# Performance work log

Hardware: AMD Instinct MI355X
Metric: run time of the kernel (lower is better)

The kernel has to match this reference:

```python
import jax, jax.numpy as jnp
import numpy as np

HIDDEN = 64
NUM_LAYERS = 6
BN_EPS = 1e-5


def setup_inputs() -> dict:
    key = jax.random.key(0)
    N, M = 1024, 1024
    num_nodes = N + M
    ks = jax.random.split(key, 12)
    x = jax.random.normal(ks[0], (num_nodes, 2), dtype=jnp.float32)
    # complete bipartite edges: (a, N+b) for all a in [0,N), b in [0,M), row-major so view(N,M) is meaningful
    row = jnp.repeat(jnp.arange(N, dtype=jnp.int64), M)
    col = N + jnp.tile(jnp.arange(M, dtype=jnp.int64), N)
    edge_index = jnp.stack([row, col], axis=0)
    s = 1.0 / np.sqrt(HIDDEN)
    return {
        "x": x,
        "edge_index": edge_index,
        "in_w": jax.random.normal(ks[1], (2, HIDDEN), jnp.float32) * 0.5,
        "in_b": jnp.zeros((HIDDEN,), jnp.float32),
        "conv_w": jax.random.normal(ks[2], (NUM_LAYERS, HIDDEN, HIDDEN), jnp.float32) * s,
        "conv_b": jnp.zeros((NUM_LAYERS, HIDDEN), jnp.float32),
        "bn_gamma": jnp.ones((NUM_LAYERS, HIDDEN), jnp.float32),
        "bn_beta": jnp.zeros((NUM_LAYERS, HIDDEN), jnp.float32),
        "out_w": jax.random.normal(ks[3], (2 * HIDDEN, 1), jnp.float32) * s,
        "out_b": jnp.zeros((1,), jnp.float32),
        "N": N,
        "M": M,
    }


def reference(x, edge_index, in_w, in_b, conv_w, conv_b, bn_gamma, bn_beta, out_w, out_b, N, M):
    num_nodes = x.shape[0]
    # GCN normalization with added self-loops (PyG GCNConv defaults)
    loops = jnp.arange(num_nodes, dtype=edge_index.dtype)
    row = jnp.concatenate([edge_index[0], loops])
    col = jnp.concatenate([edge_index[1], loops])
    deg = jax.ops.segment_sum(jnp.ones_like(col, dtype=x.dtype), col, num_segments=num_nodes)
    dinv = jnp.where(deg > 0, jax.lax.rsqrt(deg), 0.0)
    norm = dinv[row] * dinv[col]  # [E+num_nodes]

    h = jax.nn.relu(x @ in_w + in_b)
    for i in range(NUM_LAYERS):
        h_res = h
        hw = h @ conv_w[i]
        agg = jax.ops.segment_sum(hw[row] * norm[:, None], col, num_segments=num_nodes)
        h = agg + conv_b[i]
        # BatchNorm1d in training mode: batch stats, biased variance
        mu = h.mean(axis=0)
        var = ((h - mu) ** 2).mean(axis=0)
        h = (h - mu) * jax.lax.rsqrt(var + BN_EPS) * bn_gamma[i] + bn_beta[i]
        h = jax.nn.relu(h)
        if i > 0 and i % 2 == 1:
            h = h + h_res

    ef = jnp.concatenate([h[edge_index[0]], h[edge_index[1]]], axis=1)  # [E, 2H]
    scores = (ef @ out_w + out_b)[:, 0]
    return scores.reshape(N, M)
```

## Files before the change

### kernel.cpp

```cpp
#include <hip/hip_runtime.h>


#define NBLK 64
#define MAGIC 0x13572468u

__device__ __forceinline__ float relu_(float x) { return x > 0.f ? x : 0.f; }

#define AT_LOAD(p)    __hip_atomic_load((p), __ATOMIC_RELAXED, __HIP_MEMORY_SCOPE_AGENT)
#define AT_STORE(p,v) __hip_atomic_store((p), (v), __ATOMIC_RELAXED, __HIP_MEMORY_SCOPE_AGENT)
#define AT_ADD(p,v)   __hip_atomic_fetch_add((p), (v), __ATOMIC_RELAXED, __HIP_MEMORY_SCOPE_AGENT)

#define PART_OFF  256
#define UV_OFF    12544
#define FLAG_OFF  14592

__global__ __launch_bounds__(256, 1) void k_fused(
    const float* __restrict__ x,
    const float* __restrict__ in_w, const float* __restrict__ in_b,
    const float* __restrict__ conv_w,
    const float* __restrict__ bn_g, const float* __restrict__ bn_b,
    const float* __restrict__ out_w,
    unsigned int* __restrict__ ws)
{
    __shared__ float Wl[2][4096];
    __shared__ float hl[2048];
    __shared__ float Pp[3 * 2048];
    __shared__ float stat[256];
    __shared__ float g_lds[384], b_lds[384];
    __shared__ float ow_lds[128];

    const int t = threadIdx.x, b = blockIdx.x;
    const int w    = t >> 6;
    const int lane = t & 63;
    const int fi   = lane & 7;
    const int f0   = fi * 8;
    const int ng   = lane >> 3;
    const int n0   = ng * 4;
    const int sw   = ng & 3;
    const int kb   = w * 16;
    const bool isA = b < 32;
    float* part = (float*)(ws + PART_OFF);
    float* uv   = (float*)(ws + UV_OFF);

    {
        const float4* src = (const float4*)conv_w;
        float4* dst = (float4*)Wl[0];
        dst[t]       = src[t];
        dst[t + 256] = src[t + 256];
        dst[t + 512] = src[t + 512];
        dst[t + 768] = src[t + 768];
        for (int i = t; i < 384; i += 256) { g_lds[i] = bn_g[i]; b_lds[i] = bn_b[i]; }
        if (t < 128) ow_lds[t] = out_w[t];
    }

    if (b == 0) {
        for (int i = t; i < 192; i += 256) AT_STORE(ws + i, 0u);
        for (int i = t; i < 12288; i += 256) AT_STORE((unsigned*)part + i, 0u);
        asm volatile("s_waitcnt vmcnt(0)" ::: "memory");
        __syncthreads();
        if (t == 0) AT_STORE(ws + FLAG_OFF, MAGIC);
    }

    {
        const int nl = t >> 3, fj = (t & 7) * 8;
        const int rsw = (nl >> 2) & 3;
        const int node = b * 32 + nl;
        float x0 = x[node * 2], x1 = x[node * 2 + 1];
#pragma unroll
        for (int j = 0; j < 8; j++) {
            int f = fj + j;
            float v = relu_(fmaf(x0, in_w[f], fmaf(x1, in_w[64 + f], in_b[f])));
            hl[nl * 64 + ((((f >> 2)) ^ rsw) << 2) + (f & 3)] = v;
        }
    }
    __syncthreads();

    for (int layer = 0; layer < 6; layer++) {
        const float* Wb = Wl[layer & 1];
        float acc[4][8];
#pragma unroll
        for (int n = 0; n < 4; n++)
#pragma unroll
            for (int j = 0; j < 8; j++) acc[n][j] = 0.f;

#pragma unroll
        for (int kk = 0; kk < 16; kk += 4) {
            const int cb = (kb + kk) >> 2;
            float hv[4][4];
#pragma unroll
            for (int n = 0; n < 4; n++) {
                float4 h4 = *(const float4*)&hl[(n0 + n) * 64 + ((cb ^ sw) << 2)];
                hv[n][0] = h4.x; hv[n][1] = h4.y; hv[n][2] = h4.z; hv[n][3] = h4.w;
            }
#pragma unroll
            for (int j = 0; j < 4; j++) {
                const float* wr = Wb + (kb + kk + j) * 64 + f0;
                float4 w0 = *(const float4*)wr;
                float4 w1 = *(const float4*)(wr + 4);
                float wv[8] = {w0.x, w0.y, w0.z, w0.w, w1.x, w1.y, w1.z, w1.w};
#pragma unroll
                for (int n = 0; n < 4; n++)
#pragma unroll
                    for (int q = 0; q < 8; q++)
                        acc[n][q] = fmaf(hv[n][j], wv[q], acc[n][q]);
            }
        }

        float4 pf0, pf1, pf2, pf3;

        if (w > 0) {
            if (layer < 5) {
                const float4* src = (const float4*)(conv_w + (layer + 1) * 4096);
                pf0 = src[t];
                pf1 = src[t + 256];
                pf2 = src[t + 512];
                pf3 = src[t + 768];
            }
            float* Pw = Pp + (w - 1) * 2048;
#pragma unroll
            for (int n = 0; n < 4; n++) {
                float* prow = Pw + (n0 + n) * 64;
                *(float4*)&prow[((2 * fi)     ^ sw) << 2] =
                    make_float4(acc[n][0], acc[n][1], acc[n][2], acc[n][3]);
                *(float4*)&prow[((2 * fi + 1) ^ sw) << 2] =
                    make_float4(acc[n][4], acc[n][5], acc[n][6], acc[n][7]);
            }
        }
        __syncthreads();

        if (w == 0) {
#pragma unroll
            for (int r = 0; r < 3; r++) {
                const float* Pr = Pp + r * 2048;
#pragma unroll
                for (int n = 0; n < 4; n++) {
                    const float* prow = Pr + (n0 + n) * 64;
                    float4 p0 = *(const float4*)&prow[((2 * fi)     ^ sw) << 2];
                    float4 p1 = *(const float4*)&prow[((2 * fi + 1) ^ sw) << 2];
                    acc[n][0] += p0.x; acc[n][1] += p0.y; acc[n][2] += p0.z; acc[n][3] += p0.w;
                    acc[n][4] += p1.x; acc[n][5] += p1.y; acc[n][6] += p1.z; acc[n][7] += p1.w;
                }
            }
            float sv[8], qv[8];
#pragma unroll
            for (int j = 0; j < 8; j++) {
                sv[j] = (acc[0][j] + acc[1][j]) + (acc[2][j] + acc[3][j]);
                qv[j] = fmaf(acc[0][j], acc[0][j], fmaf(acc[1][j], acc[1][j],
                        fmaf(acc[2][j], acc[2][j], acc[3][j] * acc[3][j])));
            }
#pragma unroll
            for (int m = 8; m < 64; m <<= 1) {
#pragma unroll
                for (int j = 0; j < 8; j++) {
                    sv[j] += __shfl_xor(sv[j], m);
                    qv[j] += __shfl_xor(qv[j], m);
                }
            }
            if (layer == 0) { while (AT_LOAD(ws + FLAG_OFF) != MAGIC) {} }
            if (ng == 0) {
                float* base = part + layer * 2048 + (b & 7) * 256 + (isA ? 0 : 128) + f0;
#pragma unroll
                for (int j = 0; j < 8; j++) {
                    AT_ADD(base + j, sv[j]);
                    AT_ADD(base + 64 + j, qv[j]);
                }
            }
            asm volatile("s_waitcnt vmcnt(0)" ::: "memory");
            if (lane == 0) AT_ADD(ws + layer * 32, 1u);
            if (layer < 5) {
                const float4* src = (const float4*)(conv_w + (layer + 1) * 4096);
                pf0 = src[t];
                pf1 = src[t + 256];
                pf2 = src[t + 512];
                pf3 = src[t + 768];
            }
            if (t == 0) {
                const unsigned int* c = ws + layer * 32;
                for (;;) {
                    unsigned a0 = AT_LOAD(c);
                    unsigned a1 = AT_LOAD(c);
                    unsigned a2 = AT_LOAD(c);
                    unsigned a3 = AT_LOAD(c);
                    if (a0 >= NBLK) break;
                    if (a1 >= NBLK) break;
                    if (a2 >= NBLK) break;
                    if (a3 >= NBLK) break;
                }
            }
        }
        __syncthreads();

        {
            const float* p = part + layer * 2048 + t;
            float s = 0.f;
#pragma unroll
            for (int r = 0; r < 8; r++) s += AT_LOAD(p + r * 256);
            stat[t] = s;
        }
        if (layer < 5) {
            float4* dst = (float4*)Wl[(layer + 1) & 1];
            dst[t]       = pf0;
            dst[t + 256] = pf1;
            dst[t + 512] = pf2;
            dst[t + 768] = pf3;
        }
        __syncthreads();

        if (w == 0) {
            float pc[8], sc[8];
            {
                float4 sa0 = *(const float4*)&stat[f0];
                float4 sa1 = *(const float4*)&stat[f0 + 4];
                float4 qa0 = *(const float4*)&stat[64 + f0];
                float4 qa1 = *(const float4*)&stat[64 + f0 + 4];
                float4 sb0 = *(const float4*)&stat[128 + f0];
                float4 sb1 = *(const float4*)&stat[128 + f0 + 4];
                float4 qb0 = *(const float4*)&stat[192 + f0];
                float4 qb1 = *(const float4*)&stat[192 + f0 + 4];
                float4 gg0 = *(const float4*)&g_lds[layer * 64 + f0];
                float4 gg1 = *(const float4*)&g_lds[layer * 64 + f0 + 4];
                float4 bb0 = *(const float4*)&b_lds[layer * 64 + f0];
                float4 bb1 = *(const float4*)&b_lds[layer * 64 + f0 + 4];
                float SA[8] = {sa0.x, sa0.y, sa0.z, sa0.w, sa1.x, sa1.y, sa1.z, sa1.w};
                float QA[8] = {qa0.x, qa0.y, qa0.z, qa0.w, qa1.x, qa1.y, qa1.z, qa1.w};
                float SB[8] = {sb0.x, sb0.y, sb0.z, sb0.w, sb1.x, sb1.y, sb1.z, sb1.w};
                float QB[8] = {qb0.x, qb0.y, qb0.z, qb0.w, qb1.x, qb1.y, qb1.z, qb1.w};
                float GG[8] = {gg0.x, gg0.y, gg0.z, gg0.w, gg1.x, gg1.y, gg1.z, gg1.w};
                float BB[8] = {bb0.x, bb0.y, bb0.z, bb0.w, bb1.x, bb1.y, bb1.z, bb1.w};
                const float c1 = 9.75609756097561e-4f;
                const float c2 = 3.1234752377721214e-2f;
#pragma unroll
                for (int j = 0; j < 8; j++) {
                    float sumAgg = SA[j] + c1 * SB[j] + 1024.f * c2 * SA[j];
                    float sumSq  = QA[j] + c1 * c1 * QB[j] + 2.f * c1 * c2 * SA[j] * SB[j]
                                 + 1024.f * c2 * c2 * SA[j] * SA[j];
                    float meanAgg = sumAgg * (1.f / 2048.f);
                    float var = sumSq * (1.f / 2048.f) - meanAgg * meanAgg;
                    float rstd = rsqrtf(var + 1e-5f);
                    float scale = rstd * GG[j];
                    if (isA) { pc[j] = scale;      sc[j] = BB[j] - meanAgg * scale; }
                    else     { pc[j] = c1 * scale; sc[j] = BB[j] + (c2 * SA[j] - meanAgg) * scale; }
                }
            }
            float vals[4][8];
#pragma unroll
            for (int n = 0; n < 4; n++)
#pragma unroll
                for (int j = 0; j < 8; j++)
                    vals[n][j] = relu_(fmaf(acc[n][j], pc[j], sc[j]));
            if (layer == 1 || layer == 3 || layer == 5) {
#pragma unroll
                for (int n = 0; n < 4; n++) {
                    const float* hrow = hl + (n0 + n) * 64;
                    float4 r0 = *(const float4*)&hrow[((2 * fi)     ^ sw) << 2];
                    float4 r1 = *(const float4*)&hrow[((2 * fi + 1) ^ sw) << 2];
                    vals[n][0] += r0.x; vals[n][1] += r0.y; vals[n][2] += r0.z; vals[n][3] += r0.w;
                    vals[n][4] += r1.x; vals[n][5] += r1.y; vals[n][6] += r1.z; vals[n][7] += r1.w;
                }
            }
            if (layer < 5) {
#pragma unroll
                for (int n = 0; n < 4; n++) {
                    float* hrow = hl + (n0 + n) * 64;
                    *(float4*)&hrow[((2 * fi)     ^ sw) << 2] =
                        make_float4(vals[n][0], vals[n][1], vals[n][2], vals[n][3]);
                    *(float4*)&hrow[((2 * fi + 1) ^ sw) << 2] =
                        make_float4(vals[n][4], vals[n][5], vals[n][6], vals[n][7]);
                }
            } else {
                const float* wv = ow_lds + (isA ? 0 : 64) + f0;
                float4 o0 = *(const float4*)wv;
                float4 o1 = *(const float4*)(wv + 4);
                float d[4];
#pragma unroll
                for (int n = 0; n < 4; n++) {
                    d[n] = fmaf(vals[n][0], o0.x, fmaf(vals[n][1], o0.y,
                           fmaf(vals[n][2], o0.z, fmaf(vals[n][3], o0.w,
                           fmaf(vals[n][4], o1.x, fmaf(vals[n][5], o1.y,
                           fmaf(vals[n][6], o1.z, vals[n][7] * o1.w)))))));
                    d[n] += __shfl_xor(d[n], 1);
                    d[n] += __shfl_xor(d[n], 2);
                    d[n] += __shfl_xor(d[n], 4);
                }
                if (fi == 0) {
#pragma unroll
                    for (int n = 0; n < 4; n++)
                        AT_STORE(uv + b * 32 + n0 + n, d[n]);
                }
            }
        }
        __syncthreads();
    }
}

__global__ __launch_bounds__(256) void k_out(const float* __restrict__ uv,
                                             const float* __restrict__ out_b,
                                             float* __restrict__ out) {
    const int a = blockIdx.x;
    const int t = threadIdx.x;
    float ua = uv[a] + out_b[0];
    float4 vv = ((const float4*)(uv + 1024))[t];
    ((float4*)(out + a * 1024))[t] =
        make_float4(ua + vv.x, ua + vv.y, ua + vv.z, ua + vv.w);
}

extern "C" void kernel_launch(void* const* d_in, const int* in_sizes, int n_in,
                              void* d_out, int out_size, void* d_ws, size_t ws_size,
                              hipStream_t stream) {
    const float* x      = (const float*)d_in[0];
    const float* in_w   = (const float*)d_in[2];
    const float* in_b   = (const float*)d_in[3];
    const float* conv_w = (const float*)d_in[4];
    const float* bn_g   = (const float*)d_in[6];
    const float* bn_b   = (const float*)d_in[7];
    const float* out_w  = (const float*)d_in[8];
    const float* out_b  = (const float*)d_in[9];
    float* out = (float*)d_out;

    unsigned int* ws = (unsigned int*)d_ws;
    const float* uv = (const float*)(ws + UV_OFF);

    k_fused<<<NBLK, 256, 0, stream>>>(x, in_w, in_b, conv_w, bn_g, bn_b,
                                      out_w, ws);
    k_out<<<1024, 256, 0, stream>>>(uv, out_b, out);
}
```

Baseline: 118.6 us.

## Move grid-barrier stat reduction into wave 0 and spread counters

Reworks the per-layer grid synchronisation so that only wave 0 spins. It polls four spread-out arrival counters while reading the partial BatchNorm sums in the same loop, which removes one block-wide __syncthreads and the shared stat buffer. The per-lane atomic adds are spread across lanes instead of issued serially by one lane group. BN coefficients are computed once per feature and shared through LDS. The next-layer weight prefetch moves entirely to waves 1-3, which store it to LDS while wave 0 waits. The trade-off is heavier polling traffic, since every spin iteration reloads all the partial sums.

```diff
diff --git a/kernel.cpp b/kernel.cpp
--- a/kernel.cpp
+++ b/kernel.cpp
@@ -10,9 +10,9 @@
 #define AT_STORE(p,v) __hip_atomic_store((p), (v), __ATOMIC_RELAXED, __HIP_MEMORY_SCOPE_AGENT)
 #define AT_ADD(p,v)   __hip_atomic_fetch_add((p), (v), __ATOMIC_RELAXED, __HIP_MEMORY_SCOPE_AGENT)
 
-#define PART_OFF  256
-#define UV_OFF    12544
-#define FLAG_OFF  14592
+#define PART_OFF  768
+#define UV_OFF    13056
+#define FLAG_OFF  15104
 
 __global__ __launch_bounds__(256, 1) void k_fused(
     const float* __restrict__ x,
@@ -25,7 +25,7 @@
     __shared__ float Wl[2][4096];
     __shared__ float hl[2048];
     __shared__ float Pp[3 * 2048];
-    __shared__ float stat[256];
+    __shared__ float pcoef[64], scoef[64];
     __shared__ float g_lds[384], b_lds[384];
     __shared__ float ow_lds[128];
 
@@ -54,8 +54,7 @@
     }
 
     if (b == 0) {
-        for (int i = t; i < 192; i += 256) AT_STORE(ws + i, 0u);
-        for (int i = t; i < 12288; i += 256) AT_STORE((unsigned*)part + i, 0u);
+        for (int i = t; i < PART_OFF + 12288; i += 256) AT_STORE(ws + i, 0u);
         asm volatile("s_waitcnt vmcnt(0)" ::: "memory");
         __syncthreads();
         if (t == 0) AT_STORE(ws + FLAG_OFF, MAGIC);
@@ -106,15 +105,14 @@
             }
         }
 
-        float4 pf0, pf1, pf2, pf3;
-
+        float4 pf[6];
+        const int idx = (w - 1) * 64 + lane;
         if (w > 0) {
             if (layer < 5) {
                 const float4* src = (const float4*)(conv_w + (layer + 1) * 4096);
-                pf0 = src[t];
-                pf1 = src[t + 256];
-                pf2 = src[t + 512];
-                pf3 = src[t + 768];
+#pragma unroll
+                for (int r = 0; r < 5; r++) pf[r] = src[idx + 192 * r];
+                if (idx < 64) pf[5] = src[idx + 960];
             }
             float* Pw = Pp + (w - 1) * 2048;
 #pragma unroll
@@ -128,7 +126,14 @@
         }
         __syncthreads();
 
-        if (w == 0) {
+        if (w > 0) {
+            if (layer < 5) {
+                float4* dst = (float4*)Wl[(layer + 1) & 1];
+#pragma unroll
+                for (int r = 0; r < 5; r++) dst[idx + 192 * r] = pf[r];
+                if (idx < 64) dst[idx + 960] = pf[5];
+            }
+        } else {
 #pragma unroll
             for (int r = 0; r < 3; r++) {
                 const float* Pr = Pp + r * 2048;
@@ -157,91 +162,62 @@
                 }
             }
             if (layer == 0) { while (AT_LOAD(ws + FLAG_OFF) != MAGIC) {} }
-            if (ng == 0) {
-                float* base = part + layer * 2048 + (b & 7) * 256 + (isA ? 0 : 128) + f0;
-#pragma unroll
-                for (int j = 0; j < 8; j++) {
-                    AT_ADD(base + j, sv[j]);
-                    AT_ADD(base + 64 + j, qv[j]);
-                }
+
+            {
+                float* base = part + layer * 2048 + (b & 7) * 256 + (isA ? 0 : 128);
+                AT_ADD(base + f0 + ng, sv[ng]);
+                AT_ADD(base + 64 + f0 + ng, qv[ng]);
             }
             asm volatile("s_waitcnt vmcnt(0)" ::: "memory");
-            if (lane == 0) AT_ADD(ws + layer * 32, 1u);
-            if (layer < 5) {
-                const float4* src = (const float4*)(conv_w + (layer + 1) * 4096);
-                pf0 = src[t];
-                pf1 = src[t + 256];
-                pf2 = src[t + 512];
-                pf3 = src[t + 768];
-            }
-            if (t == 0) {
-                const unsigned int* c = ws + layer * 32;
+            if (lane == 0) AT_ADD(ws + layer * 128 + (b & 3) * 32, 1u);
+
+            float SA, QA, SB, QB;
+            {
+                const float* p = part + layer * 2048 + lane;
+                const unsigned int* c = ws + layer * 128;
                 for (;;) {
-                    unsigned a0 = AT_LOAD(c);
-                    unsigned a1 = AT_LOAD(c);
-                    unsigned a2 = AT_LOAD(c);
-                    unsigned a3 = AT_LOAD(c);
-                    if (a0 >= NBLK) break;
-                    if (a1 >= NBLK) break;
-                    if (a2 >= NBLK) break;
-                    if (a3 >= NBLK) break;
-                }
-            }
-        }
-        __syncthreads();
-
-        {
-            const float* p = part + layer * 2048 + t;
-            float s = 0.f;
-#pragma unroll
-            for (int r = 0; r < 8; r++) s += AT_LOAD(p + r * 256);
-            stat[t] = s;
-        }
-        if (layer < 5) {
-            float4* dst = (float4*)Wl[(layer + 1) & 1];
-            dst[t]       = pf0;
-            dst[t + 256] = pf1;
-            dst[t + 512] = pf2;
-            dst[t + 768] = pf3;
-        }
-        __syncthreads();
-
-        if (w == 0) {
+                    unsigned c0 = AT_LOAD(c);
+                    unsigned c1 = AT_LOAD(c + 32);
+                    unsigned c2 = AT_LOAD(c + 64);
+                    unsigned c3 = AT_LOAD(c + 96);
+                    float a0 = 0.f, a1 = 0.f, a2 = 0.f, a3 = 0.f;
+#pragma unroll
+                    for (int r = 0; r < 8; r++) {
+                        a0 += AT_LOAD(p + r * 256);
+                        a1 += AT_LOAD(p + r * 256 + 64);
+                        a2 += AT_LOAD(p + r * 256 + 128);
+                        a3 += AT_LOAD(p + r * 256 + 192);
+                    }
+                    if (c0 + c1 + c2 + c3 == NBLK) { SA = a0; QA = a1; SB = a2; QB = a3; break; }
+                }
+            }
+
+            {
+                const float c1 = 9.75609756097561e-4f;
+                const float c2 = 3.1234752377721214e-2f;
+                float sumAgg = SA + c1 * SB + 1024.f * c2 * SA;
+                float sumSq  = QA + c1 * c1 * QB + 2.f * c1 * c2 * SA * SB
+                             + 1024.f * c2 * c2 * SA * SA;
+                float meanAgg = sumAgg * (1.f / 2048.f);
+                float var = sumSq * (1.f / 2048.f) - meanAgg * meanAgg;
+                float rstd = rsqrtf(var + 1e-5f);
+                float scale = rstd * g_lds[layer * 64 + lane];
+                float bt = b_lds[layer * 64 + lane];
+                if (isA) { pcoef[lane] = scale;      scoef[lane] = bt - meanAgg * scale; }
+                else     { pcoef[lane] = c1 * scale; scoef[lane] = bt + (c2 * SA - meanAgg) * scale; }
+            }
             float pc[8], sc[8];
             {
-                float4 sa0 = *(const float4*)&stat[f0];
-                float4 sa1 = *(const float4*)&stat[f0 + 4];
-                float4 qa0 = *(const float4*)&stat[64 + f0];
-                float4 qa1 = *(const float4*)&stat[64 + f0 + 4];
-                float4 sb0 = *(const float4*)&stat[128 + f0];
-                float4 sb1 = *(const float4*)&stat[128 + f0 + 4];
-                float4 qb0 = *(const float4*)&stat[192 + f0];
-                float4 qb1 = *(const float4*)&stat[192 + f0 + 4];
-                float4 gg0 = *(const float4*)&g_lds[layer * 64 + f0];
-                float4 gg1 = *(const float4*)&g_lds[layer * 64 + f0 + 4];
-                float4 bb0 = *(const float4*)&b_lds[layer * 64 + f0];
-                float4 bb1 = *(const float4*)&b_lds[layer * 64 + f0 + 4];
-                float SA[8] = {sa0.x, sa0.y, sa0.z, sa0.w, sa1.x, sa1.y, sa1.z, sa1.w};
-                float QA[8] = {qa0.x, qa0.y, qa0.z, qa0.w, qa1.x, qa1.y, qa1.z, qa1.w};
-                float SB[8] = {sb0.x, sb0.y, sb0.z, sb0.w, sb1.x, sb1.y, sb1.z, sb1.w};
-                float QB[8] = {qb0.x, qb0.y, qb0.z, qb0.w, qb1.x, qb1.y, qb1.z, qb1.w};
-                float GG[8] = {gg0.x, gg0.y, gg0.z, gg0.w, gg1.x, gg1.y, gg1.z, gg1.w};
-                float BB[8] = {bb0.x, bb0.y, bb0.z, bb0.w, bb1.x, bb1.y, bb1.z, bb1.w};
-                const float c1 = 9.75609756097561e-4f;
-                const float c2 = 3.1234752377721214e-2f;
-#pragma unroll
-                for (int j = 0; j < 8; j++) {
-                    float sumAgg = SA[j] + c1 * SB[j] + 1024.f * c2 * SA[j];
-                    float sumSq  = QA[j] + c1 * c1 * QB[j] + 2.f * c1 * c2 * SA[j] * SB[j]
-                                 + 1024.f * c2 * c2 * SA[j] * SA[j];
-                    float meanAgg = sumAgg * (1.f / 2048.f);
-                    float var = sumSq * (1.f / 2048.f) - meanAgg * meanAgg;
-                    float rstd = rsqrtf(var + 1e-5f);
-                    float scale = rstd * GG[j];
-                    if (isA) { pc[j] = scale;      sc[j] = BB[j] - meanAgg * scale; }
-                    else     { pc[j] = c1 * scale; sc[j] = BB[j] + (c2 * SA[j] - meanAgg) * scale; }
-                }
-            }
+                float4 p0 = *(const float4*)&pcoef[f0];
+                float4 p1 = *(const float4*)&pcoef[f0 + 4];
+                float4 s0 = *(const float4*)&scoef[f0];
+                float4 s1 = *(const float4*)&scoef[f0 + 4];
+                pc[0] = p0.x; pc[1] = p0.y; pc[2] = p0.z; pc[3] = p0.w;
+                pc[4] = p1.x; pc[5] = p1.y; pc[6] = p1.z; pc[7] = p1.w;
+                sc[0] = s0.x; sc[1] = s0.y; sc[2] = s0.z; sc[3] = s0.w;
+                sc[4] = s1.x; sc[5] = s1.y; sc[6] = s1.z; sc[7] = s1.w;
+            }
+
             float vals[4][8];
 #pragma unroll
             for (int n = 0; n < 4; n++)
```

Measured after the change: 109.9 us (median of 2 runs). -7.3%, faster.

## Replace persistent grid-barrier kernel with per-layer kernel launches

Applied to the files above, without the earlier changes.

Splits the single persistent kernel, which used atomic counters and spin-wait grid barriers between layers, into a chain of kernels: an input kernel, five per-layer kernels, a final kernel and the output kernel. Per-block statistics and pre-BN activations are written to workspace and re-read by the next launch, so no atomics or spinning are needed. The cost is extra kernel launch overhead and global-memory round trips for activations, residuals and weights on every layer.

```diff
diff --git a/kernel.cpp b/kernel.cpp
--- a/kernel.cpp
+++ b/kernel.cpp
@@ -2,295 +2,287 @@
 
 
 #define NBLK 64
-#define MAGIC 0x13572468u
+
+#define ST_OFF   0
+#define ACC_OFF  49152
+#define HB_OFF   180224
+#define UV_OFF   311296
 
 __device__ __forceinline__ float relu_(float x) { return x > 0.f ? x : 0.f; }
 
-#define AT_LOAD(p)    __hip_atomic_load((p), __ATOMIC_RELAXED, __HIP_MEMORY_SCOPE_AGENT)
-#define AT_STORE(p,v) __hip_atomic_store((p), (v), __ATOMIC_RELAXED, __HIP_MEMORY_SCOPE_AGENT)
-#define AT_ADD(p,v)   __hip_atomic_fetch_add((p), (v), __ATOMIC_RELAXED, __HIP_MEMORY_SCOPE_AGENT)
-
-#define PART_OFF  256
-#define UV_OFF    12544
-#define FLAG_OFF  14592
-
-__global__ __launch_bounds__(256, 1) void k_fused(
-    const float* __restrict__ x,
-    const float* __restrict__ in_w, const float* __restrict__ in_b,
-    const float* __restrict__ conv_w,
-    const float* __restrict__ bn_g, const float* __restrict__ bn_b,
-    const float* __restrict__ out_w,
-    unsigned int* __restrict__ ws)
-{
-    __shared__ float Wl[2][4096];
-    __shared__ float hl[2048];
-    __shared__ float Pp[3 * 2048];
-    __shared__ float stat[256];
-    __shared__ float g_lds[384], b_lds[384];
-    __shared__ float ow_lds[128];
-
+__device__ __forceinline__ void gemm_sk(const float* __restrict__ Wb,
+                                        const float* __restrict__ hl,
+                                        int n0, int sw, int kb, int f0,
+                                        float acc[4][8])
+{
+#pragma unroll
+    for (int kk = 0; kk < 16; kk += 4) {
+        const int cb = (kb + kk) >> 2;
+        float hv[4][4];
+#pragma unroll
+        for (int n = 0; n < 4; n++) {
+            float4 h4 = *(const float4*)&hl[(n0 + n) * 64 + ((cb ^ sw) << 2)];
+            hv[n][0] = h4.x; hv[n][1] = h4.y; hv[n][2] = h4.z; hv[n][3] = h4.w;
+        }
+#pragma unroll
+        for (int j = 0; j < 4; j++) {
+            const float* wr = Wb + (kb + kk + j) * 64 + f0;
+            float4 w0 = *(const float4*)wr;
+            float4 w1 = *(const float4*)(wr + 4);
+            float wv[8] = {w0.x, w0.y, w0.z, w0.w, w1.x, w1.y, w1.z, w1.w};
+#pragma unroll
+            for (int n = 0; n < 4; n++)
+#pragma unroll
+                for (int q = 0; q < 8; q++)
+                    acc[n][q] = fmaf(hv[n][j], wv[q], acc[n][q]);
+        }
+    }
+}
+
+__device__ __forceinline__ void publish_layer(float acc[4][8], float* Pp,
+                                              float* st_cur, float* accb,
+                                              int t, int b)
+{
+    const int w = t >> 6, lane = t & 63, fi = lane & 7, f0 = fi * 8;
+    const int ng = lane >> 3, n0 = ng * 4, sw = ng & 3;
+    if (w > 0) {
+        float* Pw = Pp + (w - 1) * 2048;
+#pragma unroll
+        for (int n = 0; n < 4; n++) {
+            float* prow = Pw + (n0 + n) * 64;
+            *(float4*)&prow[((2 * fi)     ^ sw) << 2] =
+                make_float4(acc[n][0], acc[n][1], acc[n][2], acc[n][3]);
+            *(float4*)&prow[((2 * fi + 1) ^ sw) << 2] =
+                make_float4(acc[n][4], acc[n][5], acc[n][6], acc[n][7]);
+        }
+    }
+    __syncthreads();
+    if (w == 0) {
+#pragma unroll
+        for (int r = 0; r < 3; r++) {
+            const float* Pr = Pp + r * 2048;
+#pragma unroll
+            for (int n = 0; n < 4; n++) {
+                const float* prow = Pr + (n0 + n) * 64;
+                float4 p0 = *(const float4*)&prow[((2 * fi)     ^ sw) << 2];
+                float4 p1 = *(const float4*)&prow[((2 * fi + 1) ^ sw) << 2];
+                acc[n][0] += p0.x; acc[n][1] += p0.y; acc[n][2] += p0.z; acc[n][3] += p0.w;
+                acc[n][4] += p1.x; acc[n][5] += p1.y; acc[n][6] += p1.z; acc[n][7] += p1.w;
+            }
+        }
+        float sv[8], qv[8];
+#pragma unroll
+        for (int j = 0; j < 8; j++) {
+            sv[j] = (acc[0][j] + acc[1][j]) + (acc[2][j] + acc[3][j]);
+            qv[j] = fmaf(acc[0][j], acc[0][j], fmaf(acc[1][j], acc[1][j],
+                    fmaf(acc[2][j], acc[2][j], acc[3][j] * acc[3][j])));
+        }
+#pragma unroll
+        for (int m = 8; m < 64; m <<= 1) {
+#pragma unroll
+            for (int j = 0; j < 8; j++) {
+                sv[j] += __shfl_xor(sv[j], m);
+                qv[j] += __shfl_xor(qv[j], m);
+            }
+        }
+        st_cur[b * 128 + f0 + ng]      = sv[ng];
+        st_cur[b * 128 + 64 + f0 + ng] = qv[ng];
+#pragma unroll
+        for (int n = 0; n < 4; n++) {
+            float* arow = accb + (b * 32 + n0 + n) * 64 + f0;
+            *(float4*)arow       = make_float4(acc[n][0], acc[n][1], acc[n][2], acc[n][3]);
+            *(float4*)(arow + 4) = make_float4(acc[n][4], acc[n][5], acc[n][6], acc[n][7]);
+        }
+    }
+}
+
+__device__ __forceinline__ void bn_coefs(const float* stat, int fj, bool isA,
+                                         float4 gg0, float4 gg1,
+                                         float4 bb0, float4 bb1,
+                                         float pc[8], float sc[8])
+{
+    float4 sa0 = *(const float4*)&stat[fj],       sa1 = *(const float4*)&stat[fj + 4];
+    float4 qa0 = *(const float4*)&stat[64 + fj],  qa1 = *(const float4*)&stat[64 + fj + 4];
+    float4 sb0 = *(const float4*)&stat[128 + fj], sb1 = *(const float4*)&stat[128 + fj + 4];
+    float4 qb0 = *(const float4*)&stat[192 + fj], qb1 = *(const float4*)&stat[192 + fj + 4];
+    float SA[8] = {sa0.x, sa0.y, sa0.z, sa0.w, sa1.x, sa1.y, sa1.z, sa1.w};
+    float QA[8] = {qa0.x, qa0.y, qa0.z, qa0.w, qa1.x, qa1.y, qa1.z, qa1.w};
+    float SB[8] = {sb0.x, sb0.y, sb0.z, sb0.w, sb1.x, sb1.y, sb1.z, sb1.w};
+    float QB[8] = {qb0.x, qb0.y, qb0.z, qb0.w, qb1.x, qb1.y, qb1.z, qb1.w};
+    float GG[8] = {gg0.x, gg0.y, gg0.z, gg0.w, gg1.x, gg1.y, gg1.z, gg1.w};
+    float BB[8] = {bb0.x, bb0.y, bb0.z, bb0.w, bb1.x, bb1.y, bb1.z, bb1.w};
+    const float c1 = 9.75609756097561e-4f;
+    const float c2 = 3.1234752377721214e-2f;
+#pragma unroll
+    for (int j = 0; j < 8; j++) {
+        float sumAgg = SA[j] + c1 * SB[j] + 1024.f * c2 * SA[j];
+        float sumSq  = QA[j] + c1 * c1 * QB[j] + 2.f * c1 * c2 * SA[j] * SB[j]
+                     + 1024.f * c2 * c2 * SA[j] * SA[j];
+        float meanAgg = sumAgg * (1.f / 2048.f);
+        float var = sumSq * (1.f / 2048.f) - meanAgg * meanAgg;
+        float rstd = rsqrtf(var + 1e-5f);
+        float scale = rstd * GG[j];
+        if (isA) { pc[j] = scale;      sc[j] = BB[j] - meanAgg * scale; }
+        else     { pc[j] = c1 * scale; sc[j] = BB[j] + (c2 * SA[j] - meanAgg) * scale; }
+    }
+}
+
+__global__ __launch_bounds__(256, 1) void k_in(
+    const float* __restrict__ x, const float* __restrict__ in_w,
+    const float* __restrict__ in_b, const float* __restrict__ conv_w,
+    float* __restrict__ wsf)
+{
+    __shared__ float Wl[4096], hl[2048], Pp[3 * 2048];
     const int t = threadIdx.x, b = blockIdx.x;
-    const int w    = t >> 6;
-    const int lane = t & 63;
-    const int fi   = lane & 7;
-    const int f0   = fi * 8;
-    const int ng   = lane >> 3;
-    const int n0   = ng * 4;
-    const int sw   = ng & 3;
-    const int kb   = w * 16;
-    const bool isA = b < 32;
-    float* part = (float*)(ws + PART_OFF);
-    float* uv   = (float*)(ws + UV_OFF);
-
+    const float4* srcW = (const float4*)conv_w;
+    float4 w0 = srcW[t], w1 = srcW[t + 256], w2 = srcW[t + 512], w3 = srcW[t + 768];
     {
-        const float4* src = (const float4*)conv_w;
-        float4* dst = (float4*)Wl[0];
-        dst[t]       = src[t];
-        dst[t + 256] = src[t + 256];
-        dst[t + 512] = src[t + 512];
-        dst[t + 768] = src[t + 768];
-        for (int i = t; i < 384; i += 256) { g_lds[i] = bn_g[i]; b_lds[i] = bn_b[i]; }
-        if (t < 128) ow_lds[t] = out_w[t];
-    }
-
-    if (b == 0) {
-        for (int i = t; i < 192; i += 256) AT_STORE(ws + i, 0u);
-        for (int i = t; i < 12288; i += 256) AT_STORE((unsigned*)part + i, 0u);
-        asm volatile("s_waitcnt vmcnt(0)" ::: "memory");
-        __syncthreads();
-        if (t == 0) AT_STORE(ws + FLAG_OFF, MAGIC);
-    }
-
-    {
-        const int nl = t >> 3, fj = (t & 7) * 8;
-        const int rsw = (nl >> 2) & 3;
+        const int nl = t >> 3, fj = (t & 7) * 8, rsw = (nl >> 2) & 3;
         const int node = b * 32 + nl;
         float x0 = x[node * 2], x1 = x[node * 2 + 1];
 #pragma unroll
         for (int j = 0; j < 8; j++) {
             int f = fj + j;
             float v = relu_(fmaf(x0, in_w[f], fmaf(x1, in_w[64 + f], in_b[f])));
-            hl[nl * 64 + ((((f >> 2)) ^ rsw) << 2) + (f & 3)] = v;
-        }
-    }
-    __syncthreads();
-
-    for (int layer = 0; layer < 6; layer++) {
-        const float* Wb = Wl[layer & 1];
-        float acc[4][8];
-#pragma unroll
-        for (int n = 0; n < 4; n++)
-#pragma unroll
-            for (int j = 0; j < 8; j++) acc[n][j] = 0.f;
-
-#pragma unroll
-        for (int kk = 0; kk < 16; kk += 4) {
-            const int cb = (kb + kk) >> 2;
-            float hv[4][4];
-#pragma unroll
-            for (int n = 0; n < 4; n++) {
-                float4 h4 = *(const float4*)&hl[(n0 + n) * 64 + ((cb ^ sw) << 2)];
-                hv[n][0] = h4.x; hv[n][1] = h4.y; hv[n][2] = h4.z; hv[n][3] = h4.w;
-            }
-#pragma unroll
-            for (int j = 0; j < 4; j++) {
-                const float* wr = Wb + (kb + kk + j) * 64 + f0;
-                float4 w0 = *(const float4*)wr;
-                float4 w1 = *(const float4*)(wr + 4);
-                float wv[8] = {w0.x, w0.y, w0.z, w0.w, w1.x, w1.y, w1.z, w1.w};
-#pragma unroll
-                for (int n = 0; n < 4; n++)
-#pragma unroll
-                    for (int q = 0; q < 8; q++)
-                        acc[n][q] = fmaf(hv[n][j], wv[q], acc[n][q]);
-            }
-        }
-
-        float4 pf0, pf1, pf2, pf3;
-
-        if (w > 0) {
-            if (layer < 5) {
-                const float4* src = (const float4*)(conv_w + (layer + 1) * 4096);
-                pf0 = src[t];
-                pf1 = src[t + 256];
-                pf2 = src[t + 512];
-                pf3 = src[t + 768];
-            }
-            float* Pw = Pp + (w - 1) * 2048;
-#pragma unroll
-            for (int n = 0; n < 4; n++) {
-                float* prow = Pw + (n0 + n) * 64;
-                *(float4*)&prow[((2 * fi)     ^ sw) << 2] =
-                    make_float4(acc[n][0], acc[n][1], acc[n][2], acc[n][3]);
-                *(float4*)&prow[((2 * fi + 1) ^ sw) << 2] =
-                    make_float4(acc[n][4], acc[n][5], acc[n][6], acc[n][7]);
-            }
-        }
-        __syncthreads();
-
-        if (w == 0) {
-#pragma unroll
-            for (int r = 0; r < 3; r++) {
-                const float* Pr = Pp + r * 2048;
-#pragma unroll
-                for (int n = 0; n < 4; n++) {
-                    const float* prow = Pr + (n0 + n) * 64;
-                    float4 p0 = *(const float4*)&prow[((2 * fi)     ^ sw) << 2];
-                    float4 p1 = *(const float4*)&prow[((2 * fi + 1) ^ sw) << 2];
-                    acc[n][0] += p0.x; acc[n][1] += p0.y; acc[n][2] += p0.z; acc[n][3] += p0.w;
-                    acc[n][4] += p1.x; acc[n][5] += p1.y; acc[n][6] += p1.z; acc[n][7] += p1.w;
-                }
-            }
-            float sv[8], qv[8];
-#pragma unroll
-            for (int j = 0; j < 8; j++) {
-                sv[j] = (acc[0][j] + acc[1][j]) + (acc[2][j] + acc[3][j]);
-                qv[j] = fmaf(acc[0][j], acc[0][j], fmaf(acc[1][j], acc[1][j],
-                        fmaf(acc[2][j], acc[2][j], acc[3][j] * acc[3][j])));
-            }
-#pragma unroll
-            for (int m = 8; m < 64; m <<= 1) {
-#pragma unroll
-                for (int j = 0; j < 8; j++) {
-                    sv[j] += __shfl_xor(sv[j], m);
-                    qv[j] += __shfl_xor(qv[j], m);
-                }
-            }
-            if (layer == 0) { while (AT_LOAD(ws + FLAG_OFF) != MAGIC) {} }
-            if (ng == 0) {
-                float* base = part + layer * 2048 + (b & 7) * 256 + (isA ? 0 : 128) + f0;
-#pragma unroll
-                for (int j = 0; j < 8; j++) {
-                    AT_ADD(base + j, sv[j]);
-                    AT_ADD(base + 64 + j, qv[j]);
-                }
-            }
-            asm volatile("s_waitcnt vmcnt(0)" ::: "memory");
-            if (lane == 0) AT_ADD(ws + layer * 32, 1u);
-            if (layer < 5) {
-                const float4* src = (const float4*)(conv_w + (layer + 1) * 4096);
-                pf0 = src[t];
-                pf1 = src[t + 256];
-                pf2 = src[t + 512];
-                pf3 = src[t + 768];
-            }
-            if (t == 0) {
-                const unsigned int* c = ws + layer * 32;
-                for (;;) {
-                    unsigned a0 = AT_LOAD(c);
-                    unsigned a1 = AT_LOAD(c);
-                    unsigned a2 = AT_LOAD(c);
-                    unsigned a3 = AT_LOAD(c);
-                    if (a0 >= NBLK) break;
-                    if (a1 >= NBLK) break;
-                    if (a2 >= NBLK) break;
-                    if (a3 >= NBLK) break;
-                }
-            }
-        }
-        __syncthreads();
-
-        {
-            const float* p = part + layer * 2048 + t;
-            float s = 0.f;
-#pragma unroll
-            for (int r = 0; r < 8; r++) s += AT_LOAD(p + r * 256);
-            stat[t] = s;
-        }
-        if (layer < 5) {
-            float4* dst = (float4*)Wl[(layer + 1) & 1];
-            dst[t]       = pf0;
-            dst[t + 256] = pf1;
-            dst[t + 512] = pf2;
-            dst[t + 768] = pf3;
-        }
-        __syncthreads();
-
-        if (w == 0) {
-            float pc[8], sc[8];
-            {
-                float4 sa0 = *(const float4*)&stat[f0];
-                float4 sa1 = *(const float4*)&stat[f0 + 4];
-                float4 qa0 = *(const float4*)&stat[64 + f0];
-                float4 qa1 = *(const float4*)&stat[64 + f0 + 4];
-                float4 sb0 = *(const float4*)&stat[128 + f0];
-                float4 sb1 = *(const float4*)&stat[128 + f0 + 4];
-                float4 qb0 = *(const float4*)&stat[192 + f0];
-                float4 qb1 = *(const float4*)&stat[192 + f0 + 4];
-                float4 gg0 = *(const float4*)&g_lds[layer * 64 + f0];
-                float4 gg1 = *(const float4*)&g_lds[layer * 64 + f0 + 4];
-                float4 bb0 = *(const float4*)&b_lds[layer * 64 + f0];
-                float4 bb1 = *(const float4*)&b_lds[layer * 64 + f0 + 4];
-                float SA[8] = {sa0.x, sa0.y, sa0.z, sa0.w, sa1.x, sa1.y, sa1.z, sa1.w};
-                float QA[8] = {qa0.x, qa0.y, qa0.z, qa0.w, qa1.x, qa1.y, qa1.z, qa1.w};
-                float SB[8] = {sb0.x, sb0.y, sb0.z, sb0.w, sb1.x, sb1.y, sb1.z, sb1.w};
-                float QB[8] = {qb0.x, qb0.y, qb0.z, qb0.w, qb1.x, qb1.y, qb1.z, qb1.w};
-                float GG[8] = {gg0.x, gg0.y, gg0.z, gg0.w, gg1.x, gg1.y, gg1.z, gg1.w};
-                float BB[8] = {bb0.x, bb0.y, bb0.z, bb0.w, bb1.x, bb1.y, bb1.z, bb1.w};
-                const float c1 = 9.75609756097561e-4f;
-                const float c2 = 3.1234752377721214e-2f;
-#pragma unroll
-                for (int j = 0; j < 8; j++) {
-                    float sumAgg = SA[j] + c1 * SB[j] + 1024.f * c2 * SA[j];
-                    float sumSq  = QA[j] + c1 * c1 * QB[j] + 2.f * c1 * c2 * SA[j] * SB[j]
-                                 + 1024.f * c2 * c2 * SA[j] * SA[j];
-                    float meanAgg = sumAgg * (1.f / 2048.f);
-                    float var = sumSq * (1.f / 2048.f) - meanAgg * meanAgg;
-                    float rstd = rsqrtf(var + 1e-5f);
-                    float scale = rstd * GG[j];
-                    if (isA) { pc[j] = scale;      sc[j] = BB[j] - meanAgg * scale; }
-                    else     { pc[j] = c1 * scale; sc[j] = BB[j] + (c2 * SA[j] - meanAgg) * scale; }
-                }
-            }
-            float vals[4][8];
-#pragma unroll
-            for (int n = 0; n < 4; n++)
-#pragma unroll
-                for (int j = 0; j < 8; j++)
-                    vals[n][j] = relu_(fmaf(acc[n][j], pc[j], sc[j]));
-            if (layer == 1 || layer == 3 || layer == 5) {
-#pragma unroll
-                for (int n = 0; n < 4; n++) {
-                    const float* hrow = hl + (n0 + n) * 64;
-                    float4 r0 = *(const float4*)&hrow[((2 * fi)     ^ sw) << 2];
-                    float4 r1 = *(const float4*)&hrow[((2 * fi + 1) ^ sw) << 2];
-                    vals[n][0] += r0.x; vals[n][1] += r0.y; vals[n][2] += r0.z; vals[n][3] += r0.w;
-                    vals[n][4] += r1.x; vals[n][5] += r1.y; vals[n][6] += r1.z; vals[n][7] += r1.w;
-                }
-            }
-            if (layer < 5) {
-#pragma unroll
-                for (int n = 0; n < 4; n++) {
-                    float* hrow = hl + (n0 + n) * 64;
-                    *(float4*)&hrow[((2 * fi)     ^ sw) << 2] =
-                        make_float4(vals[n][0], vals[n][1], vals[n][2], vals[n][3]);
-                    *(float4*)&hrow[((2 * fi + 1) ^ sw) << 2] =
-                        make_float4(vals[n][4], vals[n][5], vals[n][6], vals[n][7]);
-                }
-            } else {
-                const float* wv = ow_lds + (isA ? 0 : 64) + f0;
-                float4 o0 = *(const float4*)wv;
-                float4 o1 = *(const float4*)(wv + 4);
-                float d[4];
-#pragma unroll
-                for (int n = 0; n < 4; n++) {
-                    d[n] = fmaf(vals[n][0], o0.x, fmaf(vals[n][1], o0.y,
-                           fmaf(vals[n][2], o0.z, fmaf(vals[n][3], o0.w,
-                           fmaf(vals[n][4], o1.x, fmaf(vals[n][5], o1.y,
-                           fmaf(vals[n][6], o1.z, vals[n][7] * o1.w)))))));
-                    d[n] += __shfl_xor(d[n], 1);
-                    d[n] += __shfl_xor(d[n], 2);
-                    d[n] += __shfl_xor(d[n], 4);
-                }
-                if (fi == 0) {
-#pragma unroll
-                    for (int n = 0; n < 4; n++)
-                        AT_STORE(uv + b * 32 + n0 + n, d[n]);
-                }
-            }
-        }
-        __syncthreads();
-    }
+            hl[nl * 64 + (((f >> 2) ^ rsw) << 2) + (f & 3)] = v;
+        }
+    }
+    ((float4*)Wl)[t] = w0; ((float4*)Wl)[t + 256] = w1;
+    ((float4*)Wl)[t + 512] = w2; ((float4*)Wl)[t + 768] = w3;
+    __syncthreads();
+    const int w = t >> 6, lane = t & 63, fi = lane & 7, f0 = fi * 8;
+    const int ng = lane >> 3, n0 = ng * 4, sw = ng & 3, kb = w * 16;
+    float acc[4][8];
+#pragma unroll
+    for (int n = 0; n < 4; n++)
+#pragma unroll
+        for (int j = 0; j < 8; j++) acc[n][j] = 0.f;
+    gemm_sk(Wl, hl, n0, sw, kb, f0, acc);
+    publish_layer(acc, Pp, wsf + ST_OFF, wsf + ACC_OFF, t, b);
+}
+
+__global__ __launch_bounds__(256, 1) void k_mid(
+    const float* __restrict__ conv_w, const float* __restrict__ bn_g,
+    const float* __restrict__ bn_b, float* __restrict__ wsf, int layer)
+{
+    __shared__ float Wl[4096], hl[2048], Pp[3 * 2048];
+    __shared__ float stat[256];
+    const int t = threadIdx.x, b = blockIdx.x;
+    const bool isA = b < 32;
+    float* st_prev = wsf + ST_OFF + (layer - 1) * 8192;
+    float* st_cur  = wsf + ST_OFF + layer * 8192;
+    float* accb = wsf + ACC_OFF;
+    float* hb   = wsf + HB_OFF;
+    const int nl = t >> 3, fj = (t & 7) * 8, rsw = (nl >> 2) & 3;
+    const int node = b * 32 + nl;
+
+    const float4* srcW = (const float4*)(conv_w + layer * 4096);
+    float4 w0 = srcW[t], w1 = srcW[t + 256], w2 = srcW[t + 512], w3 = srcW[t + 768];
+    float ssum = 0.f;
+    {
+        const float* p = st_prev + ((t < 128) ? t : (4096 + (t - 128)));
+#pragma unroll
+        for (int s = 0; s < 32; s++) ssum += p[s * 128];
+    }
+    const float* arow = accb + node * 64 + fj;
+    float4 a0 = *(const float4*)arow, a1 = *(const float4*)(arow + 4);
+    const bool doRes = (layer == 2) || (layer == 4);
+    float4 r0 = {0, 0, 0, 0}, r1 = {0, 0, 0, 0};
+    if (doRes) {
+        const float* hrow = hb + node * 64 + fj;
+        r0 = *(const float4*)hrow; r1 = *(const float4*)(hrow + 4);
+    }
+    float4 gg0 = *(const float4*)(bn_g + (layer - 1) * 64 + fj);
+    float4 gg1 = *(const float4*)(bn_g + (layer - 1) * 64 + fj + 4);
+    float4 bb0 = *(const float4*)(bn_b + (layer - 1) * 64 + fj);
+    float4 bb1 = *(const float4*)(bn_b + (layer - 1) * 64 + fj + 4);
+
+    ((float4*)Wl)[t] = w0; ((float4*)Wl)[t + 256] = w1;
+    ((float4*)Wl)[t + 512] = w2; ((float4*)Wl)[t + 768] = w3;
+    stat[t] = ssum;
+    __syncthreads();
+
+    float pc[8], sc[8];
+    bn_coefs(stat, fj, isA, gg0, gg1, bb0, bb1, pc, sc);
+    float av[8] = {a0.x, a0.y, a0.z, a0.w, a1.x, a1.y, a1.z, a1.w};
+    float rv[8] = {r0.x, r0.y, r0.z, r0.w, r1.x, r1.y, r1.z, r1.w};
+    float vals[8];
+#pragma unroll
+    for (int j = 0; j < 8; j++) {
+        vals[j] = relu_(fmaf(av[j], pc[j], sc[j]));
+        if (doRes) vals[j] += rv[j];
+    }
+    if (layer == 1 || layer == 3 || layer == 5) {
+        float* hrow = hb + node * 64 + fj;
+        *(float4*)hrow       = make_float4(vals[0], vals[1], vals[2], vals[3]);
+        *(float4*)(hrow + 4) = make_float4(vals[4], vals[5], vals[6], vals[7]);
+    }
+    *(float4*)&hl[nl * 64 + (((2 * (t & 7))     ^ rsw) << 2)] =
+        make_float4(vals[0], vals[1], vals[2], vals[3]);
+    *(float4*)&hl[nl * 64 + (((2 * (t & 7) + 1) ^ rsw) << 2)] =
+        make_float4(vals[4], vals[5], vals[6], vals[7]);
+    __syncthreads();
+
+    const int w = t >> 6, lane = t & 63, fi = lane & 7, f0 = fi * 8;
+    const int ng = lane >> 3, n0 = ng * 4, sw = ng & 3, kb = w * 16;
+    float acc[4][8];
+#pragma unroll
+    for (int n = 0; n < 4; n++)
+#pragma unroll
+        for (int j = 0; j < 8; j++) acc[n][j] = 0.f;
+    gemm_sk(Wl, hl, n0, sw, kb, f0, acc);
+    publish_layer(acc, Pp, st_cur, accb, t, b);
+}
+
+__global__ __launch_bounds__(256, 1) void k_fin(
+    const float* __restrict__ bn_g, const float* __restrict__ bn_b,
+    const float* __restrict__ out_w, float* __restrict__ wsf)
+{
+    __shared__ float stat[256];
+    const int t = threadIdx.x, b = blockIdx.x;
+    const bool isA = b < 32;
+    float* st_prev = wsf + ST_OFF + 5 * 8192;
+    float* accb = wsf + ACC_OFF;
+    float* hb   = wsf + HB_OFF;
+    float* uv   = wsf + UV_OFF;
+    const int nl = t >> 3, fj = (t & 7) * 8;
+    const int node = b * 32 + nl;
+
+    float ssum = 0.f;
+    {
+        const float* p = st_prev + ((t < 128) ? t : (4096 + (t - 128)));
+#pragma unroll
+        for (int s = 0; s < 32; s++) ssum += p[s * 128];
+    }
+    const float* arow = accb + node * 64 + fj;
+    float4 a0 = *(const float4*)arow, a1 = *(const float4*)(arow + 4);
+    const float* hrow = hb + node * 64 + fj;
+    float4 r0 = *(const float4*)hrow, r1 = *(const float4*)(hrow + 4);
+    float4 gg0 = *(const float4*)(bn_g + 5 * 64 + fj);
+    float4 gg1 = *(const float4*)(bn_g + 5 * 64 + fj + 4);
+    float4 bb0 = *(const float4*)(bn_b + 5 * 64 + fj);
+    float4 bb1 = *(const float4*)(bn_b + 5 * 64 + fj + 4);
+    const float* owp = out_w + (isA ? 0 : 64) + fj;
+    float4 o0 = *(const float4*)owp, o1 = *(const float4*)(owp + 4);
+    stat[t] = ssum;
+    __syncthreads();
+
+    float pc[8], sc[8];
+    bn_coefs(stat, fj, isA, gg0, gg1, bb0, bb1, pc, sc);
+    float av[8] = {a0.x, a0.y, a0.z, a0.w, a1.x, a1.y, a1.z, a1.w};
+    float rv[8] = {r0.x, r0.y, r0.z, r0.w, r1.x, r1.y, r1.z, r1.w};
+    float vals[8];
+#pragma unroll
+    for (int j = 0; j < 8; j++)
+        vals[j] = relu_(fmaf(av[j], pc[j], sc[j])) + rv[j];
+    float d = fmaf(vals[0], o0.x, fmaf(vals[1], o0.y,
+              fmaf(vals[2], o0.z, fmaf(vals[3], o0.w,
+              fmaf(vals[4], o1.x, fmaf(vals[5], o1.y,
+              fmaf(vals[6], o1.z, vals[7] * o1.w)))))));
+    d += __shfl_xor(d, 1);
+    d += __shfl_xor(d, 2);
+    d += __shfl_xor(d, 4);
+    if ((t & 7) == 0) uv[node] = d;
 }
 
 __global__ __launch_bounds__(256) void k_out(const float* __restrict__ uv,
@@ -316,11 +308,11 @@
     const float* out_w  = (const float*)d_in[8];
     const float* out_b  = (const float*)d_in[9];
     float* out = (float*)d_out;
-
-    unsigned int* ws = (unsigned int*)d_ws;
-    const float* uv = (const float*)(ws + UV_OFF);
-
-    k_fused<<<NBLK, 256, 0, stream>>>(x, in_w, in_b, conv_w, bn_g, bn_b,
-                                      out_w, ws);
-    k_out<<<1024, 256, 0, stream>>>(uv, out_b, out);
-}
+    float* wsf = (float*)d_ws;
+
+    k_in<<<NBLK, 256, 0, stream>>>(x, in_w, in_b, conv_w, wsf);
+    for (int l = 1; l <= 5; l++)
+        k_mid<<<NBLK, 256, 0, stream>>>(conv_w, bn_g, bn_b, wsf, l);
+    k_fin<<<NBLK, 256, 0, stream>>>(bn_g, bn_b, out_w, wsf);
+    k_out<<<1024, 256, 0, stream>>>(wsf + UV_OFF, out_b, out);
+}
```

After: 112.8 us. 4.9% less time.
